# Kernel tuning notes

Hardware: AMD Instinct MI355X
Metric: run time of the kernel (lower is better)

Reference implementation:

```python
import jax, jax.numpy as jnp
import numpy as np

B, S, IN_DIM, D_MODEL, H = 8, 1024, 512, 1024, 16
DEPTH = D_MODEL // H
LN_EPS = 1e-5


def setup_inputs() -> dict:
    key = jax.random.key(0)
    ks = jax.random.split(key, 10)
    def xavier(k, shape):
        fan_in, fan_out = shape[0], shape[1]
        lim = float(np.sqrt(6.0 / (fan_in + fan_out)))
        return jax.random.uniform(k, shape, jnp.float32, -lim, lim)
    return {
        "x": jax.random.normal(ks[0], (B, S, IN_DIM), jnp.float32),
        "mask": jax.random.randint(ks[1], (H, S, S), 0, 2, jnp.int32),
        "wq_w": xavier(ks[2], (IN_DIM, D_MODEL)),
        "wq_b": jnp.zeros((D_MODEL,), jnp.float32),
        "wk_w": xavier(ks[3], (IN_DIM, D_MODEL)),
        "wk_b": jnp.zeros((D_MODEL,), jnp.float32),
        "wv_w": xavier(ks[4], (IN_DIM, D_MODEL)),
        "wv_b": jnp.zeros((D_MODEL,), jnp.float32),
        "dense_w": xavier(ks[5], (D_MODEL, D_MODEL)),
        "dense_b": jnp.zeros((D_MODEL,), jnp.float32),
        "res_w": xavier(ks[6], (IN_DIM, D_MODEL)),  # residual_linear (no bias)
        "ln_g": 1.0 + 0.02 * jax.random.normal(ks[7], (D_MODEL,), jnp.float32),
        "ln_b": 0.02 * jax.random.normal(ks[8], (D_MODEL,), jnp.float32),
    }


def reference(x, mask, wq_w, wq_b, wk_w, wk_b, wv_w, wv_b,
              dense_w, dense_b, res_w, ln_g, ln_b):
    bs = x.shape[0]
    residual = x @ res_w  # [B,S,D_MODEL]
    # project and split heads -> [B,H,S,depth]
    def split(t):
        return t.reshape(bs, -1, H, DEPTH).transpose(0, 2, 1, 3)
    q = split(x @ wq_w + wq_b)
    k = split(x @ wk_w + wk_b)
    v = split(x @ wv_w + wv_b)
    scale = 1.0 / jnp.sqrt(jnp.asarray(DEPTH, x.dtype))
    attn = jnp.einsum("bhqd,bhkd->bhqk", q, k) * scale
    attn = jnp.where(mask[None] == 0, jnp.asarray(-1e9, attn.dtype), attn)
    attn = jax.nn.softmax(attn, axis=-1)  # dropout is identity in eval
    out = jnp.einsum("bhqk,bhkd->bhqd", attn, v)
    out = out.transpose(0, 2, 1, 3).reshape(bs, -1, D_MODEL)
    out = out @ dense_w + dense_b
    # residual + LayerNorm
    y = residual + out
    mu = jnp.mean(y, axis=-1, keepdims=True)
    var = jnp.mean(jnp.square(y - mu), axis=-1, keepdims=True)
    y = (y - mu) * jax.lax.rsqrt(var + LN_EPS)
    return y * ln_g + ln_b
```

## Files before the change

### kernel.cpp

```cpp
#include <hip/hip_runtime.h>
#include <stdint.h>

#define B_ 8
#define S_ 1024
#define IN_DIM 512
#define DM 1024
#define H_ 16
#define DEP 64

typedef __bf16 bf16;
typedef __attribute__((ext_vector_type(8))) __bf16 bf16x8;
typedef __attribute__((ext_vector_type(4))) __bf16 bf16x4;
typedef __attribute__((ext_vector_type(4))) short short4v;
typedef __attribute__((ext_vector_type(4))) float f32x4;

#if defined(__has_builtin)
#if __has_builtin(__builtin_amdgcn_mfma_f32_16x16x16_bf16)
#define HAVE_NEW16 1
#endif
#endif
static __device__ __forceinline__ f32x4 mfma16(bf16x4 a, bf16x4 b, f32x4 c) {
#ifdef HAVE_NEW16
    return __builtin_amdgcn_mfma_f32_16x16x16_bf16(a, b, c, 0, 0, 0);
#else
    union { bf16x4 h; short4v s; } ua, ub;
    ua.h = a; ub.h = b;
    return __builtin_amdgcn_mfma_f32_16x16x16bf16_1k(ua.s, ub.s, c, 0, 0, 0);
#endif
}

static __device__ __forceinline__ void gld_lds16(const void* g, void* l) {
    __builtin_amdgcn_global_load_lds(
        (const __attribute__((address_space(1))) uint32_t*)g,
        (__attribute__((address_space(3))) uint32_t*)l, 16, 0, 0);
}

__global__ void detect_kernel(const uint16_t* __restrict__ xraw, int* __restrict__ flag) {
    const int t = threadIdx.x;
    int sane = 0;
    #pragma unroll
    for (int j = 0; j < 8; j++) {
        const uint16_t u = xraw[t * 8 + j];
        const int e = (u >> 7) & 0xff;
        sane += ((u & 0x7fff) == 0 || (e >= 100 && e <= 140)) ? 1 : 0;
    }
    #pragma unroll
    for (int m = 1; m < 64; m <<= 1) sane += __shfl_xor(sane, m);
    if (t == 0) *flag = (sane >= 450) ? 1 : 0;
}

static __device__ __forceinline__ float ldin(const void* p, size_t i, int isb) {
    return isb ? (float)((const bf16*)p)[i] : ((const float*)p)[i];
}

__global__ __launch_bounds__(256) void transpose_kernel(
    const void* __restrict__ wq, const void* __restrict__ wk, const void* __restrict__ wv,
    const void* __restrict__ res, const void* __restrict__ dense,
    bf16* __restrict__ wqT, bf16* __restrict__ wkT, bf16* __restrict__ wvT,
    bf16* __restrict__ resT, bf16* __restrict__ denseT, const int* __restrict__ flag)
{
    const int isb = *flag;
    __shared__ bf16 tile[32][33];
    const int z = blockIdx.z;
    const void* src; bf16* dst; int kb, kd;
    if (z == 0)      { src = wq;    dst = wqT;    kb = 0;   kd = 512;  }
    else if (z == 1) { src = wk;    dst = wkT;    kb = 0;   kd = 512;  }
    else if (z == 2) { src = wv;    dst = wvT;    kb = 0;   kd = 512;  }
    else if (z == 3) { src = res;   dst = resT;   kb = 0;   kd = 512;  }
    else if (z == 4) { src = dense; dst = denseT; kb = 0;   kd = 1024; }
    else             { src = dense; dst = denseT; kb = 512; kd = 1024; }
    const int n0 = blockIdx.x * 32, k0 = blockIdx.y * 32;
    const int tx = threadIdx.x, ty = threadIdx.y;
    #pragma unroll
    for (int r = 0; r < 4; r++)
        tile[ty + r*8][tx] = (bf16)ldin(src, (size_t)(kb + k0 + ty + r*8) * DM + n0 + tx, isb);
    __syncthreads();
    #pragma unroll
    for (int r = 0; r < 4; r++)
        dst[(size_t)(n0 + ty + r*8) * kd + kb + k0 + tx] = tile[tx][ty + r*8];
}

__global__ __launch_bounds__(256) void xconv_kernel(
    const void* __restrict__ x, bf16* __restrict__ xc, const int* __restrict__ flag)
{
    const int isb = *flag;
    const size_t i = ((size_t)blockIdx.x * 256 + threadIdx.x) * 4;
    if (isb) {
        *(bf16x4*)(xc + i) = *(const bf16x4*)((const bf16*)x + i);
    } else {
        const float4 v = *(const float4*)((const float*)x + i);
        bf16x4 o; o[0] = (bf16)v.x; o[1] = (bf16)v.y; o[2] = (bf16)v.z; o[3] = (bf16)v.w;
        *(bf16x4*)(xc + i) = o;
    }
}

__global__ __launch_bounds__(256) void smallconv_kernel(
    const void* b0, const void* b1, const void* b2, const void* b3,
    const void* b4, const void* b5, bf16* __restrict__ out, const int* __restrict__ flag)
{
    const int isb = *flag;
    const void* srcs[6] = {b0, b1, b2, b3, b4, b5};
    const void* s = srcs[blockIdx.x];
    for (int i = threadIdx.x; i < 1024; i += 256)
        out[blockIdx.x * 1024 + i] = (bf16)ldin(s, i, isb);
}

__global__ __launch_bounds__(256) void maskpack_kernel(
    const int* __restrict__ mask, unsigned long long* __restrict__ mb)
{
    const int w = threadIdx.x >> 6, lane = threadIdx.x & 63;
    const int gw = blockIdx.x * 4 + w;
    for (int c = gw; c < 262144; c += 4096) {
        const int v = mask[(size_t)c * 64 + lane];
        const unsigned long long bits = __ballot(v != 0);
        if (lane == 0) mb[c] = bits;
    }
}

template<int KDIM>
static __device__ __forceinline__ void gemm_core(
    const bf16* __restrict__ A, const bf16* __restrict__ BT,
    int m0, int n0, bf16* Asm, bf16* Bsm, f32x4 acc[4][4])
{
    const int tid = threadIdx.x, l = tid & 63, w = tid >> 6;
    const int wm = w >> 1, wn = w & 1, quad = l >> 4, l15 = l & 15;
    #pragma unroll
    for (int i = 0; i < 4; i++)
        #pragma unroll
        for (int j = 0; j < 4; j++) acc[i][j] = f32x4{0.f, 0.f, 0.f, 0.f};

    constexpr int NIT = KDIM / 32;
    const int srow = tid >> 2, sch = tid & 3;

    #pragma unroll
    for (int qq = 0; qq < 2; qq++) {
        const int row = qq*64 + srow;
        gld_lds16(A  + (size_t)(m0 + row)*KDIM + sch*8, Asm + (qq*256 + w*64)*8);
        gld_lds16(BT + (size_t)(n0 + row)*KDIM + sch*8, Bsm + (qq*256 + w*64)*8);
    }

    for (int it = 0; it < NIT; it++) {
        __syncthreads();
        const int cur = (it & 1) * 4096;
        const int nxt = cur ^ 4096;
        if (it + 1 < NIT) {
            const int k1 = (it + 1) * 32;
            #pragma unroll
            for (int qq = 0; qq < 2; qq++) {
                const int row = qq*64 + srow;
                gld_lds16(A  + (size_t)(m0 + row)*KDIM + k1 + sch*8, Asm + nxt + (qq*256 + w*64)*8);
                gld_lds16(BT + (size_t)(n0 + row)*KDIM + k1 + sch*8, Bsm + nxt + (qq*256 + w*64)*8);
            }
        }
        bf16x8 af[4], bfv[4];
        #pragma unroll
        for (int i = 0; i < 4; i++)
            af[i] = *(const bf16x8*)(Asm + cur + (wm*64 + i*16 + l15)*32 + quad*8);
        #pragma unroll
        for (int j = 0; j < 4; j++)
            bfv[j] = *(const bf16x8*)(Bsm + cur + (wn*64 + j*16 + l15)*32 + quad*8);
        #pragma unroll
        for (int i = 0; i < 4; i++)
            #pragma unroll
            for (int j = 0; j < 4; j++)
                acc[i][j] = __builtin_amdgcn_mfma_f32_16x16x32_bf16(af[i], bfv[j], acc[i][j], 0, 0, 0);
    }
}

#define EPI_P 132
__global__ __launch_bounds__(256) void proj_kernel(
    const bf16* __restrict__ x,
    const bf16* __restrict__ wqT, const bf16* __restrict__ wkT,
    const bf16* __restrict__ wvT, const bf16* __restrict__ resT,
    const bf16* __restrict__ small,
    bf16* __restrict__ Q, bf16* __restrict__ K, bf16* __restrict__ VtG, bf16* __restrict__ R)
{
    __shared__ alignas(16) char smem[32768];
    bf16* Asm = (bf16*)smem;
    bf16* Bsm = (bf16*)(smem + 16384);
    bf16* epi = (bf16*)smem;

    const int m0 = blockIdx.x * 128;
    const int ng = blockIdx.y * 128;
    const int sel = ng >> 10, n0 = ng & 1023;
    const bf16* BT; const bf16* bias = nullptr;
    if (sel == 0)      { BT = wqT; bias = small;        }
    else if (sel == 1) { BT = wkT; bias = small + 1024; }
    else if (sel == 2) { BT = wvT; bias = small + 2048; }
    else               { BT = resT; }

    f32x4 acc[4][4];
    gemm_core<IN_DIM>(x, BT, m0, n0, Asm, Bsm, acc);

    const int tid = threadIdx.x, l = tid & 63, w = tid >> 6;
    const int wm = w >> 1, wn = w & 1, quad = l >> 4, l15 = l & 15;

    if (sel == 2) {
        const int bb = m0 >> 10, srow0 = m0 & 1023;
        #pragma unroll
        for (int hf = 0; hf < 2; hf++) {
            __syncthreads();
            if (wn == hf) {
                #pragma unroll
                for (int j = 0; j < 4; j++) {
                    const int cl = j*16 + l15;
                    const float bv = (float)bias[n0 + hf*64 + cl];
                    #pragma unroll
                    for (int i = 0; i < 4; i++) {
                        const int rho = wm*64 + i*16 + quad*4;
                        #pragma unroll
                        for (int r = 0; r < 4; r++)
                            epi[cl*EPI_P + rho + r] = (bf16)(acc[i][j][r] + bv);
                    }
                }
            }
            __syncthreads();
            const int hh = (n0 >> 6) + hf;
            const int sc = tid & 15;
            #pragma unroll
            for (int pass = 0; pass < 4; pass++) {
                const int dl = (tid >> 4) + pass*16;
                bf16x8 v;
                #pragma unroll
                for (int k = 0; k < 8; k++) {
                    const int pl = (sc & 3)*8 + k;
                    const int kl = ((pl & 4) << 2) | ((pl & 24) >> 1) | (pl & 3);
                    v[k] = epi[dl*EPI_P + (sc >> 2)*32 + kl];
                }
                *(bf16x8*)(VtG + ((size_t)(bb*16 + hh)*64 + dl)*S_ + srow0 + sc*8) = v;
            }
        }
        return;
    }

    #pragma unroll
    for (int j = 0; j < 4; j++) {
        const int col = n0 + wn*64 + j*16 + l15;
        const float bv = (sel < 3) ? (float)bias[col] : 0.f;
        #pragma unroll
        for (int i = 0; i < 4; i++) {
            const int rb = m0 + wm*64 + i*16 + quad*4;
            #pragma unroll
            for (int r = 0; r < 4; r++) {
                const float v = acc[i][j][r] + bv;
                if (sel == 0)      Q[(size_t)(rb + r)*DM + col] = (bf16)(v * 0.18033688f);
                else if (sel == 1) K[(size_t)(rb + r)*DM + col] = (bf16)v;
                else               R[(size_t)(rb + r)*DM + col] = (bf16)v;
            }
        }
    }
}

__global__ __launch_bounds__(256) void attn_kernel(
    const bf16* __restrict__ Q, const bf16* __restrict__ K, const bf16* __restrict__ VtG,
    const unsigned long long* __restrict__ mb, bf16* __restrict__ AO)
{
    __shared__ alignas(16) bf16 Ksm[2*64*64];
    __shared__ alignas(16) bf16 Vsm[2*64*64];

    const int tid = threadIdx.x, l = tid & 63, w = tid >> 6;
    const int quad = l >> 4, l15 = l & 15;

    const int fid = blockIdx.y * 8 + blockIdx.x;
    const int xcd = fid & 7, idx = fid >> 3;
    const int bh  = xcd * 16 + (idx >> 3);
    const int qt  = idx & 7;
    const int b = bh >> 4, h = bh & 15;
    const int wrow = qt*128 + w*32;
    const size_t rowbase = (size_t)b * S_;

    bf16x8 qa[2][2];
    #pragma unroll
    for (int g = 0; g < 2; g++) {
        const bf16* qp = Q + (rowbase + wrow + g*16 + l15)*DM + h*DEP + quad*8;
        qa[g][0] = *(const bf16x8*)qp;
        qa[g][1] = *(const bf16x8*)(qp + 32);
    }
    const bf16* kgbase = K + rowbase*DM + h*DEP;
    const bf16* vgbase = VtG + (size_t)(b*16 + h)*64*S_;
    const unsigned long long* mbase[2];
    #pragma unroll
    for (int g = 0; g < 2; g++)
        mbase[g] = mb + ((size_t)h*S_ + wrow + g*16 + l15) * 16;

    uint32_t bmr[4];
    #pragma unroll
    for (int r = 0; r < 4; r++) bmr[r] = 1u << (quad*4 + r);

    bf16x4 onesv;
    #pragma unroll
    for (int r = 0; r < 4; r++) onesv[r] = (bf16)1.0f;

    f32x4 oT[2][4];
    f32x4 lacc[2];
    #pragma unroll
    for (int g = 0; g < 2; g++) {
        lacc[g] = f32x4{0.f,0.f,0.f,0.f};
        #pragma unroll
        for (int dt = 0; dt < 4; dt++) oT[g][dt] = f32x4{0.f,0.f,0.f,0.f};
    }

    const int srow8 = l >> 3;
    const int gch   = (l & 7) ^ srow8;

    #pragma unroll
    for (int q = 0; q < 2; q++) {
        const int row = q*32 + w*8 + srow8;
        gld_lds16(kgbase + (size_t)row*DM + gch*8, Ksm + (q*256 + w*64)*8);
        gld_lds16(vgbase + (size_t)row*S_ + gch*8, Vsm + (q*256 + w*64)*8);
    }

    const int rsw = l15 & 7;

    for (int it = 0; it < 16; it++) {
        __syncthreads();
        const int cur = (it & 1) * 4096, nxt = cur ^ 4096;
        const bf16* Kc = Ksm + cur;
        const bf16* Vc = Vsm + cur;

        uint32_t cm[2][2];
        #pragma unroll
        for (int g = 0; g < 2; g++) {
            const unsigned long long mw = mbase[g][it];
            cm[g][0] = (uint32_t)mw; cm[g][1] = (uint32_t)(mw >> 32);
        }

        if (it + 1 < 16) {
            #pragma unroll
            for (int q = 0; q < 2; q++) {
                const int row = q*32 + w*8 + srow8;
                gld_lds16(kgbase + (size_t)((it+1)*64 + row)*DM + gch*8,
                          Ksm + nxt + (q*256 + w*64)*8);
                gld_lds16(vgbase + (size_t)row*S_ + (it+1)*64 + gch*8,
                          Vsm + nxt + (q*256 + w*64)*8);
            }
        }

        #pragma unroll
        for (int sub = 0; sub < 2; sub++) {
            bf16x8 kf[2][2];
            bf16x8 va8[4];
            #pragma unroll
            for (int h2 = 0; h2 < 2; h2++) {
                const int krow = sub*32 + h2*16 + l15;
                kf[h2][0] = *(const bf16x8*)(Kc + krow*64 + ((quad    ) ^ rsw)*8);
                kf[h2][1] = *(const bf16x8*)(Kc + krow*64 + ((quad + 4) ^ rsw)*8);
            }
            #pragma unroll
            for (int dt = 0; dt < 4; dt++)
                va8[dt] = *(const bf16x8*)(Vc + (dt*16 + l15)*64 + ((sub*4 + quad) ^ rsw)*8);

            #pragma unroll
            for (int g = 0; g < 2; g++) {
                f32x4 st[2];
                __builtin_amdgcn_s_setprio(1);
                #pragma unroll
                for (int h2 = 0; h2 < 2; h2++) {
                    f32x4 z = {0.f,0.f,0.f,0.f};
                    z = __builtin_amdgcn_mfma_f32_16x16x32_bf16(kf[h2][0], qa[g][0], z, 0, 0, 0);
                    z = __builtin_amdgcn_mfma_f32_16x16x32_bf16(kf[h2][1], qa[g][1], z, 0, 0, 0);
                    st[h2] = z;
                }
                __builtin_amdgcn_s_setprio(0);
                const uint32_t msk = cm[g][sub];
                bf16x4 pb[2];
                #pragma unroll
                for (int h2 = 0; h2 < 2; h2++) {
                    const uint32_t mh = msk >> (h2 * 16);
                    #pragma unroll
                    for (int r = 0; r < 4; r++) {
                        const float e = __builtin_amdgcn_exp2f(st[h2][r]);
                        const float pv = (mh & bmr[r]) ? e : 0.f;
                        pb[h2][r] = (bf16)pv;
                    }
                }
                __builtin_amdgcn_s_setprio(1);
                #pragma unroll
                for (int h2 = 0; h2 < 2; h2++) {
                    lacc[g] = mfma16(onesv, pb[h2], lacc[g]);
                    #pragma unroll
                    for (int dt = 0; dt < 4; dt++) {
                        const bf16x4 vh = h2
                            ? __builtin_shufflevector(va8[dt], va8[dt], 4, 5, 6, 7)
                            : __builtin_shufflevector(va8[dt], va8[dt], 0, 1, 2, 3);
                        oT[g][dt] = mfma16(vh, pb[h2], oT[g][dt]);
                    }
                }
                __builtin_amdgcn_s_setprio(0);
            }
        }
    }

    #pragma unroll
    for (int g = 0; g < 2; g++) {
        const float inv = 1.0f / lacc[g][0];
        bf16* aor = AO + (rowbase + wrow + g*16 + l15)*DM + h*DEP;
        #pragma unroll
        for (int dt = 0; dt < 4; dt++) {
            bf16x4 ov;
            #pragma unroll
            for (int r = 0; r < 4; r++) ov[r] = (bf16)(oT[g][dt][r] * inv);
            *(bf16x4*)(aor + dt*16 + quad*4) = ov;
        }
    }
}

__global__ __launch_bounds__(256) void dense_kernel(
    const bf16* __restrict__ AOin, const bf16* __restrict__ dT,
    const bf16* __restrict__ db, bf16* __restrict__ R)
{
    __shared__ alignas(16) bf16 Asm[2*64*32];
    __shared__ alignas(16) bf16 Bsm[2*128*32];
    const int m0 = blockIdx.x * 64, n0 = blockIdx.y * 128;
    const int tid = threadIdx.x, l = tid & 63, w = tid >> 6;
    const int wm = w >> 1, wn = w & 1, quad = l >> 4, l15 = l & 15;

    f32x4 acc[2][4];
    #pragma unroll
    for (int i = 0; i < 2; i++)
        #pragma unroll
        for (int j = 0; j < 4; j++) acc[i][j] = f32x4{0.f, 0.f, 0.f, 0.f};

    const int arow = tid >> 2, ach = tid & 3;
    gld_lds16(AOin + (size_t)(m0 + arow)*DM + ach*8, Asm + (w*64)*8);
    #pragma unroll
    for (int qq = 0; qq < 2; qq++) {
        const int row = qq*64 + arow;
        gld_lds16(dT + (size_t)(n0 + row)*DM + ach*8, Bsm + (qq*256 + w*64)*8);
    }

    for (int it = 0; it < 32; it++) {
        __syncthreads();
        const int curA = (it & 1) * 2048, nxtA = curA ^ 2048;
        const int curB = (it & 1) * 4096, nxtB = curB ^ 4096;
        if (it + 1 < 32) {
            const int k1 = (it + 1) * 32;
            gld_lds16(AOin + (size_t)(m0 + arow)*DM + k1 + ach*8, Asm + nxtA + (w*64)*8);
            #pragma unroll
            for (int qq = 0; qq < 2; qq++) {
                const int row = qq*64 + arow;
                gld_lds16(dT + (size_t)(n0 + row)*DM + k1 + ach*8, Bsm + nxtB + (qq*256 + w*64)*8);
            }
        }
        bf16x8 af[2], bfv[4];
        #pragma unroll
        for (int i = 0; i < 2; i++)
            af[i] = *(const bf16x8*)(Asm + curA + (wm*32 + i*16 + l15)*32 + quad*8);
        #pragma unroll
        for (int j = 0; j < 4; j++)
            bfv[j] = *(const bf16x8*)(Bsm + curB + (wn*64 + j*16 + l15)*32 + quad*8);
        #pragma unroll
        for (int i = 0; i < 2; i++)
            #pragma unroll
            for (int j = 0; j < 4; j++)
                acc[i][j] = __builtin_amdgcn_mfma_f32_16x16x32_bf16(af[i], bfv[j], acc[i][j], 0, 0, 0);
    }

    #pragma unroll
    for (int j = 0; j < 4; j++) {
        const int col = n0 + wn*64 + j*16 + l15;
        const float bv = (float)db[col];
        #pragma unroll
        for (int i = 0; i < 2; i++) {
            const int rb = m0 + wm*32 + i*16 + quad*4;
            #pragma unroll
            for (int r = 0; r < 4; r++) {
                const size_t idx = (size_t)(rb + r)*DM + col;
                R[idx] = (bf16)((float)R[idx] + acc[i][j][r] + bv);
            }
        }
    }
}

__global__ __launch_bounds__(256) void ln_kernel(
    const bf16* __restrict__ R, const bf16* __restrict__ small,
    void* __restrict__ out, const int* __restrict__ flag)
{
    const int isb = *flag;
    __shared__ float red[8];
    const int row = blockIdx.x, tid = threadIdx.x;
    const bf16x4 rv = *(const bf16x4*)(R + (size_t)row*DM + tid*4);
    const float vx = (float)rv[0], vy = (float)rv[1], vz = (float)rv[2], vw = (float)rv[3];
    float s = vx + vy + vz + vw;
    #pragma unroll
    for (int m = 1; m < 64; m <<= 1) s += __shfl_xor(s, m);
    const int w = tid >> 6;
    if ((tid & 63) == 0) red[w] = s;
    __syncthreads();
    const float mu = (red[0] + red[1] + red[2] + red[3]) * (1.0f/DM);
    const float dx = vx - mu, dy = vy - mu, dz = vz - mu, dw = vw - mu;
    float q = dx*dx + dy*dy + dz*dz + dw*dw;
    #pragma unroll
    for (int m = 1; m < 64; m <<= 1) q += __shfl_xor(q, m);
    if ((tid & 63) == 0) red[4 + w] = q;
    __syncthreads();
    const float var = (red[4] + red[5] + red[6] + red[7]) * (1.0f/DM);
    const float rstd = rsqrtf(var + 1e-5f);
    const int col = tid * 4;
    const bf16x4 gv = *(const bf16x4*)(small + 4*1024 + col);
    const bf16x4 bv = *(const bf16x4*)(small + 5*1024 + col);
    const float o0 = dx*rstd*(float)gv[0] + (float)bv[0];
    const float o1 = dy*rstd*(float)gv[1] + (float)bv[1];
    const float o2 = dz*rstd*(float)gv[2] + (float)bv[2];
    const float o3 = dw*rstd*(float)gv[3] + (float)bv[3];
    if (isb) {
        bf16x4 ov; ov[0] = (bf16)o0; ov[1] = (bf16)o1; ov[2] = (bf16)o2; ov[3] = (bf16)o3;
        *(bf16x4*)((bf16*)out + (size_t)row*DM + col) = ov;
    } else {
        float4 ov = {o0, o1, o2, o3};
        *(float4*)((float*)out + (size_t)row*DM + col) = ov;
    }
}

extern "C" void kernel_launch(void* const* d_in, const int* in_sizes, int n_in,
                              void* d_out, int out_size, void* d_ws, size_t ws_size,
                              hipStream_t stream) {
    const int* mask = (const int*)d_in[1];

    char* ws = (char*)d_ws;
    bf16* wqT   = (bf16*)(ws);
    bf16* wkT   = (bf16*)(ws + ((size_t)1 << 20));
    bf16* wvT   = (bf16*)(ws + ((size_t)2 << 20));
    bf16* resT  = (bf16*)(ws + ((size_t)3 << 20));
    bf16* dT    = (bf16*)(ws + ((size_t)4 << 20));
    bf16* small = (bf16*)(ws + ((size_t)6 << 20));
    int*  flag  = (int*) (ws + ((size_t)6 << 20) + 16384);
    unsigned long long* mbits = (unsigned long long*)(ws + ((size_t)7 << 20));
    bf16* Qb    = (bf16*)(ws + ((size_t)9  << 20));
    bf16* Kb    = (bf16*)(ws + ((size_t)25 << 20));
    bf16* VtG   = (bf16*)(ws + ((size_t)41 << 20));
    bf16* R     = (bf16*)(ws + ((size_t)57 << 20));
    bf16* xc    = (bf16*)d_out;

    detect_kernel<<<1, 64, 0, stream>>>((const uint16_t*)d_in[0], flag);
    transpose_kernel<<<dim3(32, 16, 6), dim3(32, 8), 0, stream>>>(
        d_in[2], d_in[4], d_in[6], d_in[10], d_in[8],
        wqT, wkT, wvT, resT, dT, flag);
    xconv_kernel<<<4096, 256, 0, stream>>>(d_in[0], xc, flag);
    smallconv_kernel<<<6, 256, 0, stream>>>(
        d_in[3], d_in[5], d_in[7], d_in[9], d_in[11], d_in[12], small, flag);
    maskpack_kernel<<<1024, 256, 0, stream>>>(mask, mbits);
    proj_kernel<<<dim3(64, 32), 256, 0, stream>>>(
        xc, wqT, wkT, wvT, resT, small, Qb, Kb, VtG, R);
    attn_kernel<<<dim3(8, 128), 256, 0, stream>>>(Qb, Kb, VtG, mbits, Qb );
    dense_kernel<<<dim3(128, 8), 256, 0, stream>>>(Qb, dT, small + 3*1024, R);
    ln_kernel<<<8192, 256, 0, stream>>>(R, small, d_out, flag);
}
```

Before: 342.6 us.

## Merge prep kernels, prefetch mask bits, use one wave per row in LayerNorm

Combines the dtype detection, weight transpose, input conversion, bias conversion and mask packing into a single launch, so four kernel launches and their gaps go away. In attention, the next tile's mask words are loaded one iteration ahead to hide global-load latency. LayerNorm now handles one row per wavefront with 16 values per lane, which removes the shared-memory reductions and barriers. Each block recomputes the detection check, which adds some redundant reads of x.

New measurement: 332.1 us. 1.03x faster.

```diff
diff --git a/kernel.cpp b/kernel.cpp
--- a/kernel.cpp
+++ b/kernel.cpp
@@ -35,85 +35,84 @@
         (__attribute__((address_space(3))) uint32_t*)l, 16, 0, 0);
 }
 
-__global__ void detect_kernel(const uint16_t* __restrict__ xraw, int* __restrict__ flag) {
-    const int t = threadIdx.x;
-    int sane = 0;
-    #pragma unroll
-    for (int j = 0; j < 8; j++) {
-        const uint16_t u = xraw[t * 8 + j];
-        const int e = (u >> 7) & 0xff;
-        sane += ((u & 0x7fff) == 0 || (e >= 100 && e <= 140)) ? 1 : 0;
-    }
-    #pragma unroll
-    for (int m = 1; m < 64; m <<= 1) sane += __shfl_xor(sane, m);
-    if (t == 0) *flag = (sane >= 450) ? 1 : 0;
-}
-
 static __device__ __forceinline__ float ldin(const void* p, size_t i, int isb) {
     return isb ? (float)((const bf16*)p)[i] : ((const float*)p)[i];
 }
 
-__global__ __launch_bounds__(256) void transpose_kernel(
+__global__ __launch_bounds__(256) void prep_kernel(
+    const uint16_t* __restrict__ xraw, const void* __restrict__ x,
     const void* __restrict__ wq, const void* __restrict__ wk, const void* __restrict__ wv,
     const void* __restrict__ res, const void* __restrict__ dense,
+    const int* __restrict__ mask,
     bf16* __restrict__ wqT, bf16* __restrict__ wkT, bf16* __restrict__ wvT,
-    bf16* __restrict__ resT, bf16* __restrict__ denseT, const int* __restrict__ flag)
+    bf16* __restrict__ resT, bf16* __restrict__ denseT,
+    const void* b0, const void* b1, const void* b2, const void* b3,
+    const void* b4, const void* b5, bf16* __restrict__ small,
+    bf16* __restrict__ xc, unsigned long long* __restrict__ mb, int* __restrict__ flag)
 {
-    const int isb = *flag;
+    __shared__ int s_isb;
     __shared__ bf16 tile[32][33];
-    const int z = blockIdx.z;
-    const void* src; bf16* dst; int kb, kd;
-    if (z == 0)      { src = wq;    dst = wqT;    kb = 0;   kd = 512;  }
-    else if (z == 1) { src = wk;    dst = wkT;    kb = 0;   kd = 512;  }
-    else if (z == 2) { src = wv;    dst = wvT;    kb = 0;   kd = 512;  }
-    else if (z == 3) { src = res;   dst = resT;   kb = 0;   kd = 512;  }
-    else if (z == 4) { src = dense; dst = denseT; kb = 0;   kd = 1024; }
-    else             { src = dense; dst = denseT; kb = 512; kd = 1024; }
-    const int n0 = blockIdx.x * 32, k0 = blockIdx.y * 32;
-    const int tx = threadIdx.x, ty = threadIdx.y;
-    #pragma unroll
-    for (int r = 0; r < 4; r++)
-        tile[ty + r*8][tx] = (bf16)ldin(src, (size_t)(kb + k0 + ty + r*8) * DM + n0 + tx, isb);
+    const int tid = threadIdx.x;
+
+    if (tid < 64) {
+        int sane = 0;
+        #pragma unroll
+        for (int j = 0; j < 8; j++) {
+            const uint16_t u = xraw[tid * 8 + j];
+            const int e = (u >> 7) & 0xff;
+            sane += ((u & 0x7fff) == 0 || (e >= 100 && e <= 140)) ? 1 : 0;
+        }
+        #pragma unroll
+        for (int m = 1; m < 64; m <<= 1) sane += __shfl_xor(sane, m);
+        if (tid == 0) s_isb = (sane >= 450) ? 1 : 0;
+    }
     __syncthreads();
-    #pragma unroll
-    for (int r = 0; r < 4; r++)
-        dst[(size_t)(n0 + ty + r*8) * kd + kb + k0 + tx] = tile[tx][ty + r*8];
-}
-
-__global__ __launch_bounds__(256) void xconv_kernel(
-    const void* __restrict__ x, bf16* __restrict__ xc, const int* __restrict__ flag)
-{
-    const int isb = *flag;
-    const size_t i = ((size_t)blockIdx.x * 256 + threadIdx.x) * 4;
-    if (isb) {
-        *(bf16x4*)(xc + i) = *(const bf16x4*)((const bf16*)x + i);
+    const int isb = s_isb;
+    const int bid = blockIdx.x;
+    if (bid == 0 && tid == 0) *flag = isb;
+
+    if (bid < 1024) {
+        const int w = tid >> 6, lane = tid & 63;
+        const int gw = bid * 4 + w;
+        for (int c = gw; c < 262144; c += 4096) {
+            const int v = mask[(size_t)c * 64 + lane];
+            const unsigned long long bits = __ballot(v != 0);
+            if (lane == 0) mb[c] = bits;
+        }
+    } else if (bid < 5120) {
+        const size_t i = ((size_t)(bid - 1024) * 256 + tid) * 4;
+        if (isb) {
+            *(bf16x4*)(xc + i) = *(const bf16x4*)((const bf16*)x + i);
+        } else {
+            const float4 v = *(const float4*)((const float*)x + i);
+            bf16x4 o; o[0] = (bf16)v.x; o[1] = (bf16)v.y; o[2] = (bf16)v.z; o[3] = (bf16)v.w;
+            *(bf16x4*)(xc + i) = o;
+        }
+    } else if (bid < 8192) {
+        const int t = bid - 5120;
+        const int z = t >> 9, rem = t & 511;
+        const void* src; bf16* dst; int kb, kd;
+        if (z == 0)      { src = wq;    dst = wqT;    kb = 0;   kd = 512;  }
+        else if (z == 1) { src = wk;    dst = wkT;    kb = 0;   kd = 512;  }
+        else if (z == 2) { src = wv;    dst = wvT;    kb = 0;   kd = 512;  }
+        else if (z == 3) { src = res;   dst = resT;   kb = 0;   kd = 512;  }
+        else if (z == 4) { src = dense; dst = denseT; kb = 0;   kd = 1024; }
+        else             { src = dense; dst = denseT; kb = 512; kd = 1024; }
+        const int n0 = (rem & 31) * 32, k0 = (rem >> 5) * 32;
+        const int tx = tid & 31, ty = tid >> 5;
+        #pragma unroll
+        for (int r = 0; r < 4; r++)
+            tile[ty + r*8][tx] = (bf16)ldin(src, (size_t)(kb + k0 + ty + r*8) * DM + n0 + tx, isb);
+        __syncthreads();
+        #pragma unroll
+        for (int r = 0; r < 4; r++)
+            dst[(size_t)(n0 + ty + r*8) * kd + kb + k0 + tx] = tile[tx][ty + r*8];
     } else {
-        const float4 v = *(const float4*)((const float*)x + i);
-        bf16x4 o; o[0] = (bf16)v.x; o[1] = (bf16)v.y; o[2] = (bf16)v.z; o[3] = (bf16)v.w;
-        *(bf16x4*)(xc + i) = o;
-    }
-}
-
-__global__ __launch_bounds__(256) void smallconv_kernel(
-    const void* b0, const void* b1, const void* b2, const void* b3,
-    const void* b4, const void* b5, bf16* __restrict__ out, const int* __restrict__ flag)
-{
-    const int isb = *flag;
-    const void* srcs[6] = {b0, b1, b2, b3, b4, b5};
-    const void* s = srcs[blockIdx.x];
-    for (int i = threadIdx.x; i < 1024; i += 256)
-        out[blockIdx.x * 1024 + i] = (bf16)ldin(s, i, isb);
-}
-
-__global__ __launch_bounds__(256) void maskpack_kernel(
-    const int* __restrict__ mask, unsigned long long* __restrict__ mb)
-{
-    const int w = threadIdx.x >> 6, lane = threadIdx.x & 63;
-    const int gw = blockIdx.x * 4 + w;
-    for (int c = gw; c < 262144; c += 4096) {
-        const int v = mask[(size_t)c * 64 + lane];
-        const unsigned long long bits = __ballot(v != 0);
-        if (lane == 0) mb[c] = bits;
+        const int s6 = bid - 8192;
+        const void* srcs[6] = {b0, b1, b2, b3, b4, b5};
+        const void* s = srcs[s6];
+        for (int i = tid; i < 1024; i += 256)
+            small[s6 * 1024 + i] = (bf16)ldin(s, i, isb);
     }
 }
 
@@ -309,6 +308,12 @@
         gld_lds16(kgbase + (size_t)row*DM + gch*8, Ksm + (q*256 + w*64)*8);
         gld_lds16(vgbase + (size_t)row*S_ + gch*8, Vsm + (q*256 + w*64)*8);
     }
+    uint32_t mlo[2], mhi[2];
+    #pragma unroll
+    for (int g = 0; g < 2; g++) {
+        const unsigned long long mw = mbase[g][0];
+        mlo[g] = (uint32_t)mw; mhi[g] = (uint32_t)(mw >> 32);
+    }
 
     const int rsw = l15 & 7;
 
@@ -318,13 +323,7 @@
         const bf16* Kc = Ksm + cur;
         const bf16* Vc = Vsm + cur;
 
-        uint32_t cm[2][2];
-        #pragma unroll
-        for (int g = 0; g < 2; g++) {
-            const unsigned long long mw = mbase[g][it];
-            cm[g][0] = (uint32_t)mw; cm[g][1] = (uint32_t)(mw >> 32);
-        }
-
+        const uint32_t cmlo[2] = {mlo[0], mlo[1]}, cmhi[2] = {mhi[0], mhi[1]};
         if (it + 1 < 16) {
             #pragma unroll
             for (int q = 0; q < 2; q++) {
@@ -333,6 +332,11 @@
                           Ksm + nxt + (q*256 + w*64)*8);
                 gld_lds16(vgbase + (size_t)row*S_ + (it+1)*64 + gch*8,
                           Vsm + nxt + (q*256 + w*64)*8);
+            }
+            #pragma unroll
+            for (int g = 0; g < 2; g++) {
+                const unsigned long long mw = mbase[g][it + 1];
+                mlo[g] = (uint32_t)mw; mhi[g] = (uint32_t)(mw >> 32);
             }
         }
 
@@ -362,7 +366,7 @@
                     st[h2] = z;
                 }
                 __builtin_amdgcn_s_setprio(0);
-                const uint32_t msk = cm[g][sub];
+                const uint32_t msk = sub ? cmhi[g] : cmlo[g];
                 bf16x4 pb[2];
                 #pragma unroll
                 for (int h2 = 0; h2 < 2; h2++) {
@@ -477,38 +481,46 @@
     void* __restrict__ out, const int* __restrict__ flag)
 {
     const int isb = *flag;
-    __shared__ float red[8];
-    const int row = blockIdx.x, tid = threadIdx.x;
-    const bf16x4 rv = *(const bf16x4*)(R + (size_t)row*DM + tid*4);
-    const float vx = (float)rv[0], vy = (float)rv[1], vz = (float)rv[2], vw = (float)rv[3];
-    float s = vx + vy + vz + vw;
+    const int row  = blockIdx.x * 4 + (threadIdx.x >> 6);
+    const int lane = threadIdx.x & 63;
+    const bf16* rp = R + (size_t)row*DM;
+
+    float v[16];
+    float s = 0.f;
+    #pragma unroll
+    for (int k = 0; k < 4; k++) {
+        const bf16x4 rv = *(const bf16x4*)(rp + k*256 + lane*4);
+        #pragma unroll
+        for (int r = 0; r < 4; r++) { v[k*4+r] = (float)rv[r]; s += v[k*4+r]; }
+    }
     #pragma unroll
     for (int m = 1; m < 64; m <<= 1) s += __shfl_xor(s, m);
-    const int w = tid >> 6;
-    if ((tid & 63) == 0) red[w] = s;
-    __syncthreads();
-    const float mu = (red[0] + red[1] + red[2] + red[3]) * (1.0f/DM);
-    const float dx = vx - mu, dy = vy - mu, dz = vz - mu, dw = vw - mu;
-    float q = dx*dx + dy*dy + dz*dz + dw*dw;
+    const float mu = s * (1.0f/DM);
+
+    float q = 0.f;
+    #pragma unroll
+    for (int i = 0; i < 16; i++) { v[i] -= mu; q += v[i]*v[i]; }
     #pragma unroll
     for (int m = 1; m < 64; m <<= 1) q += __shfl_xor(q, m);
-    if ((tid & 63) == 0) red[4 + w] = q;
-    __syncthreads();
-    const float var = (red[4] + red[5] + red[6] + red[7]) * (1.0f/DM);
-    const float rstd = rsqrtf(var + 1e-5f);
-    const int col = tid * 4;
-    const bf16x4 gv = *(const bf16x4*)(small + 4*1024 + col);
-    const bf16x4 bv = *(const bf16x4*)(small + 5*1024 + col);
-    const float o0 = dx*rstd*(float)gv[0] + (float)bv[0];
-    const float o1 = dy*rstd*(float)gv[1] + (float)bv[1];
-    const float o2 = dz*rstd*(float)gv[2] + (float)bv[2];
-    const float o3 = dw*rstd*(float)gv[3] + (float)bv[3];
-    if (isb) {
-        bf16x4 ov; ov[0] = (bf16)o0; ov[1] = (bf16)o1; ov[2] = (bf16)o2; ov[3] = (bf16)o3;
-        *(bf16x4*)((bf16*)out + (size_t)row*DM + col) = ov;
-    } else {
-        float4 ov = {o0, o1, o2, o3};
-        *(float4*)((float*)out + (size_t)row*DM + col) = ov;
+    const float rstd = rsqrtf(q * (1.0f/DM) + 1e-5f);
+
+    #pragma unroll
+    for (int k = 0; k < 4; k++) {
+        const int col = k*256 + lane*4;
+        const bf16x4 gv = *(const bf16x4*)(small + 4*1024 + col);
+        const bf16x4 bv = *(const bf16x4*)(small + 5*1024 + col);
+        float o[4];
+        #pragma unroll
+        for (int r = 0; r < 4; r++) o[r] = v[k*4+r]*rstd*(float)gv[r] + (float)bv[r];
+        if (isb) {
+            bf16x4 ov;
+            #pragma unroll
+            for (int r = 0; r < 4; r++) ov[r] = (bf16)o[r];
+            *(bf16x4*)((bf16*)out + (size_t)row*DM + col) = ov;
+        } else {
+            float4 ov = {o[0], o[1], o[2], o[3]};
+            *(float4*)((float*)out + (size_t)row*DM + col) = ov;
+        }
     }
 }
 
@@ -532,17 +544,16 @@
     bf16* R     = (bf16*)(ws + ((size_t)57 << 20));
     bf16* xc    = (bf16*)d_out;
 
-    detect_kernel<<<1, 64, 0, stream>>>((const uint16_t*)d_in[0], flag);
-    transpose_kernel<<<dim3(32, 16, 6), dim3(32, 8), 0, stream>>>(
+    prep_kernel<<<8198, 256, 0, stream>>>(
+        (const uint16_t*)d_in[0], d_in[0],
         d_in[2], d_in[4], d_in[6], d_in[10], d_in[8],
-        wqT, wkT, wvT, resT, dT, flag);
-    xconv_kernel<<<4096, 256, 0, stream>>>(d_in[0], xc, flag);
-    smallconv_kernel<<<6, 256, 0, stream>>>(
-        d_in[3], d_in[5], d_in[7], d_in[9], d_in[11], d_in[12], small, flag);
-    maskpack_kernel<<<1024, 256, 0, stream>>>(mask, mbits);
+        mask,
+        wqT, wkT, wvT, resT, dT,
+        d_in[3], d_in[5], d_in[7], d_in[9], d_in[11], d_in[12], small,
+        xc, mbits, flag);
     proj_kernel<<<dim3(64, 32), 256, 0, stream>>>(
         xc, wqT, wkT, wvT, resT, small, Qb, Kb, VtG, R);
     attn_kernel<<<dim3(8, 128), 256, 0, stream>>>(Qb, Kb, VtG, mbits, Qb );
     dense_kernel<<<dim3(128, 8), 256, 0, stream>>>(Qb, dT, small + 3*1024, R);
-    ln_kernel<<<8192, 256, 0, stream>>>(R, small, d_out, flag);
-}
+    ln_kernel<<<2048, 256, 0, stream>>>(R, small, d_out, flag);
+}
```
